# Optimization experiments

Hardware: AMD Instinct MI355X
Metric: run time of the kernel (lower is better)

Reference implementation:

```python
import jax, jax.numpy as jnp
import numpy as np

NUM_CLASSES = 10
PGD_NUMS = 10
ALPHA = 0.15
# Hardcoded in the original module: sign vector for 10 classes
SIGN_VEC = jnp.array([-1.0] * 4 + [1.0] * 6, dtype=jnp.float32)


def setup_inputs() -> dict:
    key = jax.random.key(0)
    k1, k2, k3 = jax.random.split(key, 3)
    B = 1048576
    logit = jax.random.normal(k1, (B, NUM_CLASSES), dtype=jnp.float32)
    y = jax.random.randint(k2, (B,), 0, NUM_CLASSES, dtype=jnp.int32)
    label_freq = jax.random.randint(k3, (NUM_CLASSES,), 0, PGD_NUMS, dtype=jnp.int32)
    return {"logit": logit, "y": y, "label_freq": label_freq}


def _compute_adv(logit, y):
    # softmax over classes, then per-class mean of softmax rows (one-hot^T @ p)
    p = jax.nn.softmax(logit, axis=-1)  # [B, C]
    sum_class_logit = jax.ops.segment_sum(p, y, num_segments=NUM_CLASSES)  # [C, C]
    counts = jax.ops.segment_sum(jnp.ones(y.shape[0], dtype=logit.dtype), y,
                                 num_segments=NUM_CLASSES)  # [C]
    counts = jnp.where(counts == 0, jnp.asarray(100.0, logit.dtype), counts)
    mean_class_logit = sum_class_logit / counts[:, None]  # [C, C]
    grad = mean_class_logit - jnp.eye(NUM_CLASSES, dtype=logit.dtype)
    # Faithful to torch: norm over dim=0 (columns), then reshape(-1,1) divides row i
    col_norm = jnp.linalg.norm(grad, axis=0)  # [C]
    grad = grad / col_norm[:, None]
    grad = ALPHA * grad * SIGN_VEC[:, None].astype(logit.dtype)
    return grad[y]  # index_select along dim 0 -> [B, C]


def reference(logit, y, label_freq):
    logit_copy = logit

    def step(l, _):
        l_new = l + _compute_adv(l, y)
        return l_new, l_new

    _, logit_steps = jax.lax.scan(step, logit, None, length=PGD_NUMS)  # [P, B, C]

    # Original: logit_news = sum_i logit_steps[label_freq[i]] * (y == i)
    # Since class masks are disjoint, this is a per-sample gather of step label_freq[y[n]].
    steps_per_sample = label_freq[y]  # [B]
    B = logit.shape[0]
    logit_news = logit_steps[steps_per_sample, jnp.arange(B)]  # [B, C]

    # mean cross-entropy
    log_p = jax.nn.log_softmax(logit_news, axis=-1)
    loss_adv = -jnp.mean(jnp.take_along_axis(log_p, y[:, None].astype(jnp.int32), axis=1))
    return loss_adv, logit_news, logit_copy
```

## Files before the change

### kernel.cpp

```cpp
#include <hip/hip_runtime.h>
#include <hip/hip_cooperative_groups.h>

namespace cg = cooperative_groups;

#define PGD   10
#define ALPHA 0.15f
#define NTAB  32
#define NSUB  8

#define FTH   512
#define FSP   8
#define FTS   (FTH * FSP)

#define NTHR  256
#define SPT   4
#define TSAMP (NTHR * SPT)

#define WS_COUNTS 0
#define WS_STAB   320
#define WS_DGLOB  32320
#define WS_ZERO_N 33320

__global__ void k_init(float* __restrict__ ws, float* __restrict__ out) {
    int i = blockIdx.x * blockDim.x + threadIdx.x;
    if (i == 0) out[0] = 0.f;
    int gs = gridDim.x * blockDim.x;
    for (int k = i; k < WS_ZERO_N; k += gs) ws[k] = 0.f;
}

__device__ __forceinline__ void table_phase(
    const float* __restrict__ Sg, const float* __restrict__ counts_tab,
    const float* Dprev,
    float* shT, float* shCnt, float* shCn, float* shD_out, int tid)
{
    if (tid < 10) {
        float s = 0.f;
        #pragma unroll
        for (int k = 0; k < NTAB; ++k) s += counts_tab[k * 10 + tid];
        shCnt[tid] = (s == 0.f) ? 100.f : s;
    }
    if (tid < 100) {
        float s = 0.f;
        #pragma unroll
        for (int k = 0; k < NTAB; ++k) s += Sg[k * 100 + tid];
        shT[tid] = s;
    }
    __syncthreads();
    if (tid < 100) {
        int c = tid / 10, j = tid - c * 10;
        shT[tid] = shT[tid] / shCnt[c] - ((c == j) ? 1.f : 0.f);
    }
    __syncthreads();
    if (tid < 10) {
        float s = 0.f;
        for (int cc = 0; cc < 10; ++cc) { float g = shT[cc * 10 + tid]; s += g * g; }
        shCn[tid] = sqrtf(s);
    }
    __syncthreads();
    if (tid < 100) {
        int c = tid / 10;
        float sign = (c < 4) ? -1.f : 1.f;
        float g = shT[tid] / shCn[c] * (ALPHA * sign);
        shD_out[tid] = (Dprev ? Dprev[tid] : 0.f) + g;
    }
    __syncthreads();
}

__device__ __forceinline__ void load4(const float* __restrict__ logit,
                                      const int* __restrict__ y,
                                      int s0, int B, float* a, int* yc) {
    if (s0 + 4 <= B) {
        const float4* rp = reinterpret_cast<const float4*>(logit + (size_t)s0 * 10);
        float4 q[10];
        #pragma unroll
        for (int i = 0; i < 10; ++i) q[i] = rp[i];
        int4 yv = *reinterpret_cast<const int4*>(y + s0);
        #pragma unroll
        for (int i = 0; i < 10; ++i) {
            a[4 * i + 0] = q[i].x; a[4 * i + 1] = q[i].y;
            a[4 * i + 2] = q[i].z; a[4 * i + 3] = q[i].w;
        }
        yc[0] = yv.x; yc[1] = yv.y; yc[2] = yv.z; yc[3] = yv.w;
    } else {
        #pragma unroll
        for (int k = 0; k < 4; ++k) {
            int idx = s0 + k;
            if (idx < B) {
                yc[k] = y[idx];
                for (int j = 0; j < 10; ++j) a[k * 10 + j] = logit[(size_t)idx * 10 + j];
            } else {
                yc[k] = -1;
                for (int j = 0; j < 10; ++j) a[k * 10 + j] = 0.f;
            }
        }
    }
}

__global__ __launch_bounds__(FTH, 2) void k_fused(
    const float* __restrict__ logit, const int* __restrict__ y,
    const int* __restrict__ label_freq,
    float* __restrict__ out, float* __restrict__ ws, int B)
{
    cg::grid_group grid = cg::this_grid();

    __shared__ float tile[FTH * 20];
    __shared__ float Dall[PGD][100];
    __shared__ float shT[100];
    __shared__ float shCnt[10];
    __shared__ float shCn[10];
    __shared__ float wtab[NSUB][100];
    __shared__ float ctab[NSUB][10];
    __shared__ int   lf[10];
    __shared__ float wsum[8];

    const int tid = threadIdx.x;
    float* counts_tab = ws + WS_COUNTS;
    float* S_tab      = ws + WS_STAB;

    const size_t ftot = (size_t)B * 10;
    float* news_out = out + 1;
    float* copy_out = out + 1 + ftot;

    if (blockIdx.x == 0 && tid == 0) atomicExch(out, 0.f);
    if (tid < 10) lf[tid] = label_freq[tid];

    const int s0 = (blockIdx.x * FTH + tid) * FSP;
    float a[80];
    int   yc[8];
    load4(logit, y, s0,     B, a,      yc);
    load4(logit, y, s0 + 4, B, a + 40, yc + 4);

    {
        const size_t fbase = (size_t)blockIdx.x * (FTS * 10);
        #pragma unroll
        for (int i = 0; i < 20; ++i) {
            size_t fi = fbase + (size_t)(tid + i * FTH) * 4;
            if (fi + 4 <= ftot) {
                float4 v = *reinterpret_cast<const float4*>(logit + fi);
                *reinterpret_cast<float4*>(copy_out + fi) = v;
            } else {
                for (size_t e = fi; e < ftot; ++e) copy_out[e] = logit[e];
            }
        }
    }

    for (int t = 1; t <= PGD; ++t) {
        for (int i = tid; i < NSUB * 100; i += FTH) (&wtab[0][0])[i] = 0.f;
        if (t == 1) for (int i = tid; i < NSUB * 10; i += FTH) (&ctab[0][0])[i] = 0.f;
        __syncthreads();

        const int sub = ((tid >> 6) << 1) | (tid & 1);
        #pragma unroll
        for (int k = 0; k < FSP; ++k) {
            int c = yc[k];
            if (c < 0) continue;
            float tv[10];
            #pragma unroll
            for (int j = 0; j < 10; ++j) tv[j] = a[k * 10 + j];
            if (t >= 2) {
                #pragma unroll
                for (int j = 0; j < 10; ++j) tv[j] += Dall[t - 2][c * 10 + j];
            }
            float m = tv[0];
            #pragma unroll
            for (int j = 1; j < 10; ++j) m = fmaxf(m, tv[j]);
            float s = 0.f;
            #pragma unroll
            for (int j = 0; j < 10; ++j) { tv[j] = __expf(tv[j] - m); s += tv[j]; }
            float r = 1.f / s;
            #pragma unroll
            for (int j = 0; j < 10; ++j) unsafeAtomicAdd(&wtab[sub][c * 10 + j], tv[j] * r);
            if (t == 1) unsafeAtomicAdd(&ctab[sub][c], 1.f);
        }
        __syncthreads();

        const int tb = blockIdx.x & (NTAB - 1);
        if (tid < 100) {
            float s = 0.f;
            #pragma unroll
            for (int w = 0; w < NSUB; ++w) s += wtab[w][tid];
            unsafeAtomicAdd(&S_tab[(size_t)(t - 1) * (NTAB * 100) + (size_t)tb * 100 + tid], s);
        }
        if (t == 1 && tid < 10) {
            float s = 0.f;
            #pragma unroll
            for (int w = 0; w < NSUB; ++w) s += ctab[w][tid];
            unsafeAtomicAdd(&counts_tab[tb * 10 + tid], s);
        }
        __threadfence();
        grid.sync();
        __threadfence();

        table_phase(S_tab + (size_t)(t - 1) * (NTAB * 100), counts_tab,
                    (t >= 2) ? &Dall[t - 2][0] : nullptr,
                    shT, shCnt, shCn, &Dall[t - 1][0], tid);
    }

    float acc = 0.f;
    const size_t fbase = (size_t)blockIdx.x * (FTS * 10);
    for (int cc = 0; cc < 4; ++cc) {
        __syncthreads();
        if ((tid >> 7) == cc) {
            const int lt = tid & 127;
            #pragma unroll
            for (int k = 0; k < FSP; ++k) {
                int c = yc[k];
                if (c < 0) continue;
                int rrel = lt * FSP + k;
                int sel = lf[c];
                float nv[10];
                #pragma unroll
                for (int j = 0; j < 10; ++j) nv[j] = a[k * 10 + j] + Dall[sel][c * 10 + j];
                #pragma unroll
                for (int j = 0; j < 10; ++j) tile[rrel * 10 + j] = nv[j];
                float m = nv[0];
                #pragma unroll
                for (int j = 1; j < 10; ++j) m = fmaxf(m, nv[j]);
                float s = 0.f;
                #pragma unroll
                for (int j = 0; j < 10; ++j) s += __expf(nv[j] - m);
                acc += __logf(s) + m - nv[c];
            }
        }
        __syncthreads();
        const float4* tp = reinterpret_cast<const float4*>(tile);
        #pragma unroll
        for (int i = 0; i < 5; ++i) {
            size_t fo = fbase + (size_t)cc * (FTH * 20) + (size_t)(tid + i * FTH) * 4;
            if (fo + 4 <= ftot) {
                *reinterpret_cast<float4*>(news_out + fo) = tp[tid + i * FTH];
            } else {
                for (size_t e = fo; e < ftot; ++e) news_out[e] = tile[(e - fbase - (size_t)cc * (FTH * 20))];
            }
        }
    }

    #pragma unroll
    for (int off = 32; off > 0; off >>= 1) acc += __shfl_down(acc, off);
    if ((tid & 63) == 0) wsum[tid >> 6] = acc;
    __syncthreads();
    if (tid == 0) {
        float b = 0.f;
        #pragma unroll
        for (int w = 0; w < 8; ++w) b += wsum[w];
        unsafeAtomicAdd(out, b / (float)B);
    }
}

__global__ __launch_bounds__(NTHR) void k_step(
    const float* __restrict__ logit, const int* __restrict__ y,
    float* __restrict__ ws, int B, int t)
{
    __shared__ float sh_D[100];
    __shared__ float shT[100];
    __shared__ float shCnt[10];
    __shared__ float shCn[10];
    __shared__ float wtab[NSUB][100];
    __shared__ float ctab[NSUB][10];

    const int tid = threadIdx.x;
    float* counts_tab = ws + WS_COUNTS;
    float* S_tab      = ws + WS_STAB;
    float* D_glob     = ws + WS_DGLOB;

    const int s0 = (blockIdx.x * NTHR + tid) * SPT;
    float a[40];
    int   yc[4];
    load4(logit, y, s0, B, a, yc);

    for (int i = tid; i < NSUB * 100; i += NTHR) (&wtab[0][0])[i] = 0.f;
    if (t == 1) for (int i = tid; i < NSUB * 10; i += NTHR) (&ctab[0][0])[i] = 0.f;

    if (t >= 2) {
        table_phase(S_tab + (size_t)(t - 2) * (NTAB * 100), counts_tab,
                    (t >= 3) ? (D_glob + (size_t)(t - 3) * 100) : nullptr,
                    shT, shCnt, shCn, sh_D, tid);
        if (blockIdx.x == 0 && tid < 100) D_glob[(size_t)(t - 2) * 100 + tid] = sh_D[tid];
    }
    __syncthreads();

    const int sub = ((tid >> 6) << 1) | (tid & 1);
    #pragma unroll
    for (int k = 0; k < SPT; ++k) {
        int c = yc[k];
        if (c < 0) continue;
        float tv[10];
        #pragma unroll
        for (int j = 0; j < 10; ++j) tv[j] = a[k * 10 + j];
        if (t >= 2) {
            #pragma unroll
            for (int j = 0; j < 10; ++j) tv[j] += sh_D[c * 10 + j];
        }
        float m = tv[0];
        #pragma unroll
        for (int j = 1; j < 10; ++j) m = fmaxf(m, tv[j]);
        float s = 0.f;
        #pragma unroll
        for (int j = 0; j < 10; ++j) { tv[j] = __expf(tv[j] - m); s += tv[j]; }
        float r = 1.f / s;
        #pragma unroll
        for (int j = 0; j < 10; ++j) unsafeAtomicAdd(&wtab[sub][c * 10 + j], tv[j] * r);
        if (t == 1) unsafeAtomicAdd(&ctab[sub][c], 1.f);
    }
    __syncthreads();

    const int tb = blockIdx.x & (NTAB - 1);
    if (tid < 100) {
        float s = 0.f;
        #pragma unroll
        for (int w = 0; w < NSUB; ++w) s += wtab[w][tid];
        unsafeAtomicAdd(&S_tab[(size_t)(t - 1) * (NTAB * 100) + (size_t)tb * 100 + tid], s);
    }
    if (t == 1 && tid < 10) {
        float s = 0.f;
        #pragma unroll
        for (int w = 0; w < NSUB; ++w) s += ctab[w][tid];
        unsafeAtomicAdd(&counts_tab[tb * 10 + tid], s);
    }
}

__global__ __launch_bounds__(NTHR) void k_final(
    const float* __restrict__ logit, const int* __restrict__ y,
    const int* __restrict__ label_freq,
    float* __restrict__ out, float* __restrict__ ws, int B)
{
    __shared__ float tile_f[TSAMP * 10];
    __shared__ int   yt[TSAMP];
    __shared__ float Dall[PGD][100];
    __shared__ float shT[100];
    __shared__ float shCnt[10];
    __shared__ float shCn[10];
    __shared__ int   lf[10];
    __shared__ float wsum[4];

    const int tid = threadIdx.x;
    float* counts_tab = ws + WS_COUNTS;
    float* S_tab      = ws + WS_STAB;
    float* D_glob     = ws + WS_DGLOB;

    const size_t fbase = (size_t)blockIdx.x * (TSAMP * 10);
    const size_t ftot  = (size_t)B * 10;
    float4 q[10];
    int4 yq;
    #pragma unroll
    for (int i = 0; i < 10; ++i) {
        size_t fi = fbase + (size_t)(tid + i * NTHR) * 4;
        if (fi + 4 <= ftot) {
            q[i] = *reinterpret_cast<const float4*>(logit + fi);
        } else {
            float e[4];
            #pragma unroll
            for (int e2 = 0; e2 < 4; ++e2) e[e2] = (fi + e2 < ftot) ? logit[fi + e2] : 0.f;
            q[i] = make_float4(e[0], e[1], e[2], e[3]);
        }
    }
    {
        int yi = blockIdx.x * TSAMP + tid * 4;
        if (yi + 4 <= B) {
            yq = *reinterpret_cast<const int4*>(y + yi);
        } else {
            yq.x = (yi < B) ? y[yi] : 0;
            yq.y = (yi + 1 < B) ? y[yi + 1] : 0;
            yq.z = (yi + 2 < B) ? y[yi + 2] : 0;
            yq.w = (yi + 3 < B) ? y[yi + 3] : 0;
        }
    }

    table_phase(S_tab + (size_t)9 * (NTAB * 100), counts_tab, D_glob + 8 * 100,
                shT, shCnt, shCn, &Dall[9][0], tid);
    for (int i = tid; i < 900; i += NTHR) Dall[i / 100][i % 100] = D_glob[i];
    if (tid < 10) lf[tid] = label_freq[tid];

    float4* tp = reinterpret_cast<float4*>(tile_f);
    #pragma unroll
    for (int i = 0; i < 10; ++i) tp[tid + i * NTHR] = q[i];
    reinterpret_cast<int4*>(yt)[tid] = yq;
    __syncthreads();

    const int vfloat = (int)((ftot - fbase < (size_t)(TSAMP * 10)) ? (ftot - fbase)
                                                                   : (size_t)(TSAMP * 10));
    float* news_out = out + 1;
    float* copy_out = out + 1 + ftot;

    for (int m = tid; m < vfloat; m += NTHR) copy_out[fbase + m] = tile_f[m];
    __syncthreads();

    float acc = 0.f;
    #pragma unroll
    for (int k = 0; k < SPT; ++k) {
        int sl = tid + k * NTHR;
        int gi = blockIdx.x * TSAMP + sl;
        if (gi >= B) break;
        int c = yt[sl];
        int sel = lf[c];
        float2* rp = reinterpret_cast<float2*>(tile_f + sl * 10);
        float nv[10];
        #pragma unroll
        for (int h = 0; h < 5; ++h) {
            float2 v = rp[h];
            nv[2 * h]     = v.x + Dall[sel][c * 10 + 2 * h];
            nv[2 * h + 1] = v.y + Dall[sel][c * 10 + 2 * h + 1];
        }
        #pragma unroll
        for (int h = 0; h < 5; ++h) rp[h] = make_float2(nv[2 * h], nv[2 * h + 1]);
        float m = nv[0];
        #pragma unroll
        for (int j = 1; j < 10; ++j) m = fmaxf(m, nv[j]);
        float s = 0.f;
        #pragma unroll
        for (int j = 0; j < 10; ++j) s += __expf(nv[j] - m);
        acc += __logf(s) + m - nv[c];
    }
    __syncthreads();

    for (int m = tid; m < vfloat; m += NTHR) news_out[fbase + m] = tile_f[m];

    #pragma unroll
    for (int off = 32; off > 0; off >>= 1) acc += __shfl_down(acc, off);
    if ((tid & 63) == 0) wsum[tid >> 6] = acc;
    __syncthreads();
    if (tid == 0)
        unsafeAtomicAdd(out, (wsum[0] + wsum[1] + wsum[2] + wsum[3]) / (float)B);
}

extern "C" void kernel_launch(void* const* d_in, const int* in_sizes, int n_in,
                              void* d_out, int out_size, void* d_ws, size_t ws_size,
                              hipStream_t stream) {
    const float* logit = (const float*)d_in[0];
    const int*   yy    = (const int*)d_in[1];
    const int*   lf    = (const int*)d_in[2];
    float* out = (float*)d_out;
    float* ws  = (float*)d_ws;
    int B = in_sizes[0] / 10;

    int fblocks = (B + FTS - 1) / FTS;

    int dev = 0; hipGetDevice(&dev);
    int numCU = 0;
    hipDeviceGetAttribute(&numCU, hipDeviceAttributeMultiprocessorCount, dev);
    int maxB = 0;
    hipOccupancyMaxActiveBlocksPerMultiprocessor(&maxB, (const void*)k_fused, FTH, 0);
    bool coop_ok = (maxB > 0) && ((long)maxB * (long)numCU >= (long)fblocks);

    hipLaunchKernelGGL(k_init, dim3(64), dim3(256), 0, stream, ws, out);

    if (coop_ok) {
        void* args[] = { (void*)&logit, (void*)&yy, (void*)&lf,
                         (void*)&out, (void*)&ws, (void*)&B };
        hipLaunchCooperativeKernel((const void*)k_fused, dim3(fblocks), dim3(FTH),
                                   args, 0, stream);
    } else {
        int blocks = (B + TSAMP - 1) / TSAMP;
        for (int t = 1; t <= PGD; ++t)
            hipLaunchKernelGGL(k_step, dim3(blocks), dim3(NTHR), 0, stream,
                               logit, yy, ws, B, t);
        hipLaunchKernelGGL(k_final, dim3(blocks), dim3(NTHR), 0, stream,
                           logit, yy, lf, out, ws, B);
    }
}
```

Before: 645.7 us.

## Replace cooperative grid sync with custom atomic barrier and halve samples per thread

Replaces cg::grid.sync with a hand-written global counter barrier (an atomic fetch-add, then a spin with s_sleep) and reads the reduction tables with relaxed agent-scope atomic loads. It also cuts the samples per thread from 8 to 4, which doubles the grid size and lowers register pressure. The goal is cheaper grid-wide synchronisation across the ten PGD steps and more blocks for latency hiding. In exchange there are more blocks contending on the shared atomics and the barrier counter, and the barrier is only correct if all blocks are co-resident.

```diff
diff --git a/kernel.cpp b/kernel.cpp
--- a/kernel.cpp
+++ b/kernel.cpp
@@ -1,7 +1,5 @@
 #include <hip/hip_runtime.h>
 #include <hip/hip_cooperative_groups.h>
-
-namespace cg = cooperative_groups;
 
 #define PGD   10
 #define ALPHA 0.15f
@@ -9,7 +7,7 @@
 #define NSUB  8
 
 #define FTH   512
-#define FSP   8
+#define FSP   4
 #define FTS   (FTH * FSP)
 
 #define NTHR  256
@@ -19,7 +17,8 @@
 #define WS_COUNTS 0
 #define WS_STAB   320
 #define WS_DGLOB  32320
-#define WS_ZERO_N 33320
+#define WS_BAR    33320
+#define WS_ZERO_N 33324
 
 __global__ void k_init(float* __restrict__ ws, float* __restrict__ out) {
     int i = blockIdx.x * blockDim.x + threadIdx.x;
@@ -28,10 +27,14 @@
     for (int k = i; k < WS_ZERO_N; k += gs) ws[k] = 0.f;
 }
 
+__device__ __forceinline__ float aload(const float* p) {
+    return __hip_atomic_load(p, __ATOMIC_RELAXED, __HIP_MEMORY_SCOPE_AGENT);
+}
+
 __device__ __forceinline__ void table_phase(
     const float* __restrict__ Sg, const float* __restrict__ counts_tab,
-    const float* Dprev,
-    float* shT, float* shCnt, float* shCn, float* shD_out, int tid)
+    const float* Dprev, float* shT, float* shCnt, float* shCn,
+    float* shD_out, int tid)
 {
     if (tid < 10) {
         float s = 0.f;
@@ -101,9 +104,7 @@
     const int* __restrict__ label_freq,
     float* __restrict__ out, float* __restrict__ ws, int B)
 {
-    cg::grid_group grid = cg::this_grid();
-
-    __shared__ float tile[FTH * 20];
+    __shared__ float tile[1024 * 10];
     __shared__ float Dall[PGD][100];
     __shared__ float shT[100];
     __shared__ float shCnt[10];
@@ -116,33 +117,32 @@
     const int tid = threadIdx.x;
     float* counts_tab = ws + WS_COUNTS;
     float* S_tab      = ws + WS_STAB;
+    int*   bar        = (int*)(ws + WS_BAR);
 
     const size_t ftot = (size_t)B * 10;
     float* news_out = out + 1;
     float* copy_out = out + 1 + ftot;
 
-    if (blockIdx.x == 0 && tid == 0) atomicExch(out, 0.f);
     if (tid < 10) lf[tid] = label_freq[tid];
 
     const int s0 = (blockIdx.x * FTH + tid) * FSP;
-    float a[80];
-    int   yc[8];
-    load4(logit, y, s0,     B, a,      yc);
-    load4(logit, y, s0 + 4, B, a + 40, yc + 4);
-
-    {
-        const size_t fbase = (size_t)blockIdx.x * (FTS * 10);
-        #pragma unroll
-        for (int i = 0; i < 20; ++i) {
-            size_t fi = fbase + (size_t)(tid + i * FTH) * 4;
-            if (fi + 4 <= ftot) {
-                float4 v = *reinterpret_cast<const float4*>(logit + fi);
-                *reinterpret_cast<float4*>(copy_out + fi) = v;
-            } else {
-                for (size_t e = fi; e < ftot; ++e) copy_out[e] = logit[e];
-            }
-        }
-    }
+    float a[40];
+    int   yc[4];
+    load4(logit, y, s0, B, a, yc);
+
+    const size_t fbase = (size_t)blockIdx.x * (FTS * 10);
+    #pragma unroll
+    for (int i = 0; i < 10; ++i) {
+        size_t fi = fbase + (size_t)(tid + i * FTH) * 4;
+        if (fi + 4 <= ftot) {
+            float4 v = *reinterpret_cast<const float4*>(logit + fi);
+            *reinterpret_cast<float4*>(copy_out + fi) = v;
+        } else {
+            for (size_t e = fi; e < ftot; ++e) copy_out[e] = logit[e];
+        }
+    }
+
+    const int nblk = gridDim.x;
 
     for (int t = 1; t <= PGD; ++t) {
         for (int i = tid; i < NSUB * 100; i += FTH) (&wtab[0][0])[i] = 0.f;
@@ -179,29 +179,62 @@
             float s = 0.f;
             #pragma unroll
             for (int w = 0; w < NSUB; ++w) s += wtab[w][tid];
-            unsafeAtomicAdd(&S_tab[(size_t)(t - 1) * (NTAB * 100) + (size_t)tb * 100 + tid], s);
+            atomicAdd(&S_tab[(size_t)(t - 1) * (NTAB * 100) + (size_t)tb * 100 + tid], s);
         }
         if (t == 1 && tid < 10) {
             float s = 0.f;
             #pragma unroll
             for (int w = 0; w < NSUB; ++w) s += ctab[w][tid];
-            unsafeAtomicAdd(&counts_tab[tb * 10 + tid], s);
-        }
-        __threadfence();
-        grid.sync();
-        __threadfence();
-
-        table_phase(S_tab + (size_t)(t - 1) * (NTAB * 100), counts_tab,
-                    (t >= 2) ? &Dall[t - 2][0] : nullptr,
-                    shT, shCnt, shCn, &Dall[t - 1][0], tid);
+            atomicAdd(&counts_tab[tb * 10 + tid], s);
+        }
+
+        __syncthreads();
+        if (tid == 0) {
+            __hip_atomic_fetch_add(bar, 1, __ATOMIC_ACQ_REL, __HIP_MEMORY_SCOPE_AGENT);
+            while (__hip_atomic_load(bar, __ATOMIC_ACQUIRE, __HIP_MEMORY_SCOPE_AGENT) < nblk * t)
+                __builtin_amdgcn_s_sleep(16);
+        }
+        __syncthreads();
+
+        if (tid < 10) {
+            float s = 0.f;
+            #pragma unroll
+            for (int k = 0; k < NTAB; ++k) s += aload(&counts_tab[k * 10 + tid]);
+            shCnt[tid] = (s == 0.f) ? 100.f : s;
+        }
+        if (tid < 100) {
+            float s = 0.f;
+            const float* Sg = S_tab + (size_t)(t - 1) * (NTAB * 100);
+            #pragma unroll
+            for (int k = 0; k < NTAB; ++k) s += aload(&Sg[k * 100 + tid]);
+            shT[tid] = s;
+        }
+        __syncthreads();
+        if (tid < 100) {
+            int c = tid / 10, j = tid - c * 10;
+            shT[tid] = shT[tid] / shCnt[c] - ((c == j) ? 1.f : 0.f);
+        }
+        __syncthreads();
+        if (tid < 10) {
+            float s = 0.f;
+            for (int cc = 0; cc < 10; ++cc) { float g = shT[cc * 10 + tid]; s += g * g; }
+            shCn[tid] = sqrtf(s);
+        }
+        __syncthreads();
+        if (tid < 100) {
+            int c = tid / 10;
+            float sign = (c < 4) ? -1.f : 1.f;
+            float g = shT[tid] / shCn[c] * (ALPHA * sign);
+            Dall[t - 1][tid] = ((t >= 2) ? Dall[t - 2][tid] : 0.f) + g;
+        }
+        __syncthreads();
     }
 
     float acc = 0.f;
-    const size_t fbase = (size_t)blockIdx.x * (FTS * 10);
-    for (int cc = 0; cc < 4; ++cc) {
-        __syncthreads();
-        if ((tid >> 7) == cc) {
-            const int lt = tid & 127;
+    for (int cc = 0; cc < 2; ++cc) {
+        __syncthreads();
+        if ((tid >> 8) == cc) {
+            const int lt = tid & 255;
             #pragma unroll
             for (int k = 0; k < FSP; ++k) {
                 int c = yc[k];
@@ -226,11 +259,12 @@
         const float4* tp = reinterpret_cast<const float4*>(tile);
         #pragma unroll
         for (int i = 0; i < 5; ++i) {
-            size_t fo = fbase + (size_t)cc * (FTH * 20) + (size_t)(tid + i * FTH) * 4;
+            size_t fo = fbase + (size_t)cc * 10240 + (size_t)(tid + i * FTH) * 4;
             if (fo + 4 <= ftot) {
                 *reinterpret_cast<float4*>(news_out + fo) = tp[tid + i * FTH];
             } else {
-                for (size_t e = fo; e < ftot; ++e) news_out[e] = tile[(e - fbase - (size_t)cc * (FTH * 20))];
+                size_t lbase = fbase + (size_t)cc * 10240;
+                for (size_t e = fo; e < ftot; ++e) news_out[e] = tile[e - lbase];
             }
         }
     }
@@ -243,7 +277,7 @@
         float b = 0.f;
         #pragma unroll
         for (int w = 0; w < 8; ++w) b += wsum[w];
-        unsafeAtomicAdd(out, b / (float)B);
+        atomicAdd(out, b / (float)B);
     }
 }
 
```

Result: no change. 645.4 us (-0.0%).
